# Kernel tuning notes

Measured on AMD Instinct MI355X. Metric: run time of the kernel, lower is better.

## Reference

```python
import jax, jax.numpy as jnp
import numpy as np

N_CLASSES = 10   # number of distinct private-attribute labels
DIM = 16         # PCA / GMM dimension (init arg `dim`)
SIGMA = 1.0      # init arg `sigma`, cov = sigma * I


def _pca(X, k):
    # torch PCA: center, SVD of X^T, project onto first k left singular vectors
    X = X - jnp.mean(X, axis=0)
    U, _, _ = jnp.linalg.svd(X.T, full_matrices=False)  # U: [D, min(D,B)]
    return X @ U[:, :k]                                  # [B, k]


def _gmm_loss(x, labels):
    # x: [B, k] PCA-projected features, labels: [B] int class ids in [0, C)
    B = x.shape[0]
    dtype = x.dtype
    ones = jnp.ones((B,), dtype)
    counts = jax.ops.segment_sum(ones, labels, num_segments=N_CLASSES)          # [C]
    sums = jax.ops.segment_sum(x, labels, num_segments=N_CLASSES)               # [C, k]
    safe = jnp.maximum(counts, 1.0)
    means = sums / safe[:, None]                                                # [C, k]

    diff = x - means[labels]                                                    # [B, k]
    outers = diff[:, :, None] * diff[:, None, :]                                # [B, k, k]
    Ssum = jax.ops.segment_sum(outers, labels, num_segments=N_CLASSES)          # [C, k, k]
    Sigma = SIGMA * jnp.eye(DIM, dtype=dtype) + Ssum / safe[:, None, None]      # [C, k, k]

    inv = jnp.linalg.inv(Sigma)                                                 # [C, k, k]
    _, logdet = jnp.linalg.slogdet(Sigma)                                       # [C]

    # KL(N_i || N_j) = 0.5*(tr(S_j^-1 S_i) + (u_j-u_i)^T S_j^-1 (u_j-u_i) - k + logdet_j - logdet_i)
    tr = jnp.einsum('jab,iba->ij', inv, Sigma)                                  # [C, C]
    d = means[None, :, :] - means[:, None, :]                                   # d[i,j] = u_j - u_i
    maha = jnp.einsum('ija,jab,ijb->ij', d, inv, d)                             # [C, C]
    kl = 0.5 * (tr + maha - DIM + logdet[None, :] - logdet[:, None])            # [C, C]

    present = counts > 0
    W = counts[:, None] * counts[None, :]
    mask = present[:, None] & present[None, :] & ~jnp.eye(N_CLASSES, dtype=bool)
    result = jnp.sum(jnp.where(mask, kl * W, jnp.zeros_like(kl)))
    return result / (jnp.asarray(B, dtype) ** 3)


def setup_inputs() -> dict:
    key = jax.random.key(0)
    k1, k2 = jax.random.split(key)
    mu = jax.random.normal(k1, (16384, 1024), dtype=jnp.float32)
    private_attribute = jax.random.randint(k2, (16384,), 0, N_CLASSES, dtype=jnp.int32)
    return {"mu": mu, "private_attribute": private_attribute}


def reference(mu, private_attribute):
    B = mu.shape[0]
    x = mu.reshape(B, -1)          # flatten(start_dim=1)
    x = _pca(x, DIM)               # [B, DIM]
    labels = private_attribute.astype(jnp.int32)
    return _gmm_loss(x, labels)
```

## Files before the change

kernel.cpp:

```cpp
#include <hip/hip_runtime.h>
#include <math.h>

#define BN 16384
#define DN 1024
#define CHEB_D 8

static constexpr size_t OFF_C    = 0x000000;
static constexpr size_t OFF_P    = 0x400000;
static constexpr size_t OFF_Y0   = 0x800000;
static constexpr size_t OFF_Y1   = 0x840000;
static constexpr size_t OFF_Y2   = 0x880000;
static constexpr size_t OFF_Y3   = 0x8C0000;
static constexpr size_t OFF_CQ   = 0x900000;
static constexpr size_t OFF_S64  = 0x940000;
static constexpr size_t OFF_LF   = 0x948000;
static constexpr size_t OFF_T64  = 0x950000;
static constexpr size_t OFF_V16  = 0x958000;
static constexpr size_t OFF_UT   = 0x960000;
static constexpr size_t OFF_UTT  = 0x970000;
static constexpr size_t OFF_S16  = 0x980000;
static constexpr size_t OFF_CS   = 0x980100;
static constexpr size_t OFF_TR   = 0x981100;
static constexpr size_t OFF_SCAL = 0x981200;
static constexpr size_t OFF_STAT = 0x981300;
static constexpr size_t OFF_F    = 0x990000;
static constexpr size_t OFF_M    = 0xA90000;

typedef float f32x4 __attribute__((ext_vector_type(4)));
typedef short bf16x4 __attribute__((ext_vector_type(4)));
typedef unsigned int u32x4v __attribute__((ext_vector_type(4)));


__global__ __launch_bounds__(256) void colsum_k(const float* __restrict__ X, float* __restrict__ cs){
  int b = blockIdx.x, t = threadIdx.x;
  float a0=0.f,a1=0.f,a2=0.f,a3=0.f;
  for (int r=0; r<256; ++r){
    const float4 v = *(const float4*)(X + (size_t)(b*256 + r)*1024 + t*4);
    a0 += v.x; a1 += v.y; a2 += v.z; a3 += v.w;
  }
  atomicAdd(&cs[t*4+0], a0); atomicAdd(&cs[t*4+1], a1);
  atomicAdd(&cs[t*4+2], a2); atomicAdd(&cs[t*4+3], a3);
}

#define SYRK_SLICES 27
#define SYRK_KCHUNK 608

__device__ __forceinline__ f32x4 mfma_bf16(bf16x4 a, bf16x4 b, f32x4 c){
  return __builtin_amdgcn_mfma_f32_16x16x16bf16_1k(a, b, c, 0, 0, 0);
}

__global__ __launch_bounds__(256, 2) void syrk_mfma_k(const float* __restrict__ X, float* __restrict__ G){
  int bx = blockIdx.x;
  int tp = bx % 36, ks = bx / 36;
  int ti = 0, rem = tp;
  while (rem >= 8 - ti){ rem -= 8 - ti; ++ti; }
  int tj = ti + rem;
  int k0 = ks * SYRK_KCHUNK;
  int kend = k0 + SYRK_KCHUNK; if (kend > 16384) kend = 16384;

  __shared__ __attribute__((aligned(16))) unsigned int LdsT[2][3][128][20];

  int t = threadIdx.x;
  int wid = t >> 6, lane = t & 63;
  int wr = wid >> 1, wc = wid & 1;
  int lm = lane & 15;
  int lk = lane >> 4;

  f32x4 acc[4][4];
  #pragma unroll
  for (int i=0;i<4;++i)
    #pragma unroll
    for (int j=0;j<4;++j) acc[i][j] = (f32x4){0.f,0.f,0.f,0.f};

  for (int kc = k0; kc < kend; kc += 32){
    __syncthreads();
    #pragma unroll
    for (int w=0; w<4; ++w){
      int job = t + 256*w;
      int c   = job & 127;
      int pk  = job >> 7;
      int p   = pk >> 2;
      int kpg = pk & 3;
      const float* src = X + (size_t)(kc + kpg*8)*1024 + (p ? tj : ti)*128 + c;
      float e[8];
      #pragma unroll
      for (int i=0;i<8;++i) e[i] = src[(size_t)i*1024];
      unsigned hh[8]; float r2f[8]; unsigned mm[8];
      #pragma unroll
      for (int i=0;i<8;++i){
        unsigned u = __float_as_uint(e[i]);
        hh[i] = u & 0xFFFF0000u;
        float r1 = e[i] - __uint_as_float(hh[i]);
        mm[i] = __float_as_uint(r1) & 0xFFFF0000u;
        r2f[i] = r1 - __uint_as_float(mm[i]);
      }
      u32x4v hp, mp, lp;
      #pragma unroll
      for (int j=0;j<4;++j){
        hp[j] = (hh[2*j] >> 16) | hh[2*j+1];
        mp[j] = (mm[2*j] >> 16) | mm[2*j+1];
        lp[j] = (__float_as_uint(r2f[2*j]) >> 16) | (__float_as_uint(r2f[2*j+1]) & 0xFFFF0000u);
      }
      *(u32x4v*)&LdsT[p][0][c][kpg*4] = hp;
      *(u32x4v*)&LdsT[p][1][c][kpg*4] = mp;
      *(u32x4v*)&LdsT[p][2][c][kpg*4] = lp;
    }
    __syncthreads();
    #pragma unroll
    for (int h=0; h<2; ++h){
      bf16x4 af[3][4], bg[3][4];
      #pragma unroll
      for (int fm=0; fm<4; ++fm){
        int ca = wr*64 + fm*16 + lm;
        int cb = wc*64 + fm*16 + lm;
        #pragma unroll
        for (int tm=0; tm<3; ++tm){
          af[tm][fm] = *(const bf16x4*)&LdsT[0][tm][ca][h*8 + lk*2];
          bg[tm][fm] = *(const bf16x4*)&LdsT[1][tm][cb][h*8 + lk*2];
        }
      }
      #pragma unroll
      for (int fm=0; fm<4; ++fm)
        #pragma unroll
        for (int fn=0; fn<4; ++fn){
          f32x4 a = acc[fm][fn];
          a = mfma_bf16(af[0][fm], bg[0][fn], a);
          a = mfma_bf16(af[0][fm], bg[1][fn], a);
          a = mfma_bf16(af[1][fm], bg[0][fn], a);
          a = mfma_bf16(af[0][fm], bg[2][fn], a);
          a = mfma_bf16(af[2][fm], bg[0][fn], a);
          a = mfma_bf16(af[1][fm], bg[1][fn], a);
          acc[fm][fn] = a;
        }
    }
  }
  #pragma unroll
  for (int fm=0; fm<4; ++fm){
    int gi = ti*128 + wr*64 + fm*16 + lk*4;
    #pragma unroll
    for (int fn=0; fn<4; ++fn){
      int gj = tj*128 + wc*64 + fn*16 + lm;
      #pragma unroll
      for (int rg=0; rg<4; ++rg)
        atomicAdd(&G[(size_t)(gi+rg)*1024 + gj], acc[fm][fn][rg]);
    }
  }
}

template<int KCHUNK>
__device__ __forceinline__ void syrk_body(const float* __restrict__ X, float* __restrict__ G, int KMAX){
  int bx = blockIdx.x;
  int tp = bx % 36, ks = bx / 36;
  int ti = 0, rem = tp;
  while (rem >= 8 - ti){ rem -= 8 - ti; ++ti; }
  int tj = ti + rem;
  int k0 = ks * KCHUNK;
  int kend = k0 + KCHUNK; if (kend > KMAX) kend = KMAX;
  __shared__ __attribute__((aligned(16))) float Xa[16][132];
  __shared__ __attribute__((aligned(16))) float Xb[16][132];
  int t = threadIdx.x;
  int tx = t & 15, ty = t >> 4;
  int kk0 = t >> 5, f4 = t & 31;
  const float* ba = X + (size_t)kk0*1024 + ti*128 + f4*4;
  const float* bb = X + (size_t)kk0*1024 + tj*128 + f4*4;
  float4 pa0, pa1, pb0, pb1;
  {
    size_t o = (size_t)k0*1024;
    pa0 = *(const float4*)(ba + o);
    pb0 = *(const float4*)(bb + o);
    pa1 = *(const float4*)(ba + o + 8*1024);
    pb1 = *(const float4*)(bb + o + 8*1024);
  }
  float acc[8][8];
  #pragma unroll
  for (int i=0;i<8;++i)
    #pragma unroll
    for (int j=0;j<8;++j) acc[i][j] = 0.f;
  for (int kc = k0; kc < kend; kc += 16){
    __syncthreads();
    *(float4*)&Xa[kk0][f4*4]   = pa0;
    *(float4*)&Xa[kk0+8][f4*4] = pa1;
    *(float4*)&Xb[kk0][f4*4]   = pb0;
    *(float4*)&Xb[kk0+8][f4*4] = pb1;
    __syncthreads();
    if (kc + 16 < kend){
      size_t o = (size_t)(kc+16)*1024;
      pa0 = *(const float4*)(ba + o);
      pb0 = *(const float4*)(bb + o);
      pa1 = *(const float4*)(ba + o + 8*1024);
      pb1 = *(const float4*)(bb + o + 8*1024);
    }
    #pragma unroll
    for (int kk=0; kk<16; ++kk){
      float a[8], b[8];
      *(float4*)&a[0] = *(const float4*)&Xa[kk][tx*4];
      *(float4*)&a[4] = *(const float4*)&Xa[kk][64 + tx*4];
      *(float4*)&b[0] = *(const float4*)&Xb[kk][ty*4];
      *(float4*)&b[4] = *(const float4*)&Xb[kk][64 + ty*4];
      #pragma unroll
      for (int i=0;i<8;++i)
        #pragma unroll
        for (int j=0;j<8;++j) acc[i][j] += a[i]*b[j];
    }
  }
  #pragma unroll
  for (int i=0;i<8;++i){
    int ri = ti*128 + ((i<4) ? (tx*4+i) : (64 + tx*4 + (i-4)));
    #pragma unroll
    for (int j=0;j<8;++j){
      int cj = tj*128 + ((j<4) ? (ty*4+j) : (64 + ty*4 + (j-4)));
      atomicAdd(&G[(size_t)ri*1024 + cj], acc[i][j]);
    }
  }
}

__global__ __launch_bounds__(256, 3) void syrkM_k(const float* __restrict__ X, float* __restrict__ G){
  syrk_body<128>(X, G, 1024);
}

__global__ __launch_bounds__(256) void formC_k(float* __restrict__ C, const float* __restrict__ cs, float* __restrict__ tr){
  int g = blockIdx.x*256 + threadIdx.x;
  int i = g >> 10, j = g & 1023;
  if (j < i) return;
  float v = C[g] - cs[i]*cs[j]*(1.0f/16384.0f);
  C[g] = v;
  C[j*1024 + i] = v;
  if (i == j) atomicAdd(tr, v);
}

__global__ void scal_k(const float* __restrict__ tr, float* __restrict__ scal){
  float trD = tr[0] * (1.0f/1024.0f);
  float c = 1.40f * trD, a = 0.25f * trD;
  scal[0] = 0.5f*(c + a);
  scal[1] = 2.0f/(c - a);
}

__global__ __launch_bounds__(256) void formChat_k(float* __restrict__ C, const float* __restrict__ scal){
  int g = blockIdx.x*256 + threadIdx.x;
  int i = g >> 10, j = g & 1023;
  float mid = scal[0], ie = scal[1];
  C[g] = ie*(C[g] - ((i==j) ? mid : 0.f));
}

__global__ __launch_bounds__(256) void formM_k(float* __restrict__ M){
  int g = blockIdx.x*256 + threadIdx.x;
  int i = g >> 10, j = g & 1023;
  if (j < i) return;
  float v = 2.f*M[g] - ((i==j) ? 1.f : 0.f);
  M[g] = v;
  M[j*1024 + i] = v;
}

__global__ void rng_k(float* __restrict__ Y){
  int idx = blockIdx.x*256 + threadIdx.x;
  unsigned h = (unsigned)idx * 2654435761u;
  h ^= h >> 16; h *= 2246822519u; h ^= h >> 13; h *= 3266489917u; h ^= h >> 16;
  Y[idx] = (float)(h & 0xFFFFFFu) * (2.0f/16777216.0f) - 1.0f;
}

__global__ __launch_bounds__(256) void mv_k(const float* __restrict__ Yt, const float* __restrict__ Cm, float* __restrict__ P){
  int bx = blockIdx.x;
  int nt = bx & 15, ks = bx >> 4;
  int n0 = nt*64, k0 = ks*64;
  __shared__ __attribute__((aligned(16))) float At[64][68];
  __shared__ __attribute__((aligned(16))) float Bt[64][68];
  int t = threadIdx.x;
  #pragma unroll
  for (int w=0; w<4; ++w){
    int job = t + 256*w;
    int m  = job >> 4, f4 = job & 15;
    float4 v = *(const float4*)(Yt + (size_t)m*1024 + k0 + f4*4);
    At[f4*4+0][m] = v.x; At[f4*4+1][m] = v.y; At[f4*4+2][m] = v.z; At[f4*4+3][m] = v.w;
    int kk = job >> 4, fn = job & 15;
    *(float4*)&Bt[kk][fn*4] = *(const float4*)(Cm + (size_t)(k0+kk)*1024 + n0 + fn*4);
  }
  __syncthreads();
  int tm = t & 15, tn = t >> 4;
  float acc[4][4];
  #pragma unroll
  for (int i=0;i<4;++i)
    #pragma unroll
    for (int j=0;j<4;++j) acc[i][j]=0.f;
  for (int kk=0; kk<64; ++kk){
    float4 a = *(const float4*)&At[kk][tm*4];
    float4 b = *(const float4*)&Bt[kk][tn*4];
    float av[4] = {a.x,a.y,a.z,a.w};
    float bv[4] = {b.x,b.y,b.z,b.w};
    #pragma unroll
    for (int i=0;i<4;++i)
      #pragma unroll
      for (int j=0;j<4;++j) acc[i][j] += av[i]*bv[j];
  }
  #pragma unroll
  for (int i=0;i<4;++i){
    float4 o; o.x=acc[i][0]; o.y=acc[i][1]; o.z=acc[i][2]; o.w=acc[i][3];
    *(float4*)(P + (size_t)(ks*64 + tm*4 + i)*1024 + n0 + tn*4) = o;
  }
}

__global__ __launch_bounds__(256) void combine_k(const float* __restrict__ P, const float* __restrict__ Tk1,
                                                 float* __restrict__ out, int mode){
  int idx = (blockIdx.x*256 + threadIdx.x)*4;
  float s0=0.f,s1=0.f,s2=0.f,s3=0.f;
  #pragma unroll
  for (int ks=0; ks<16; ++ks){
    const float4 p = *(const float4*)(P + (size_t)ks*65536 + idx);
    s0 += p.x; s1 += p.y; s2 += p.z; s3 += p.w;
  }
  float4 o;
  if (mode == 0){
    o.x=s0; o.y=s1; o.z=s2; o.w=s3;
  } else {
    const float4 t1 = *(const float4*)(Tk1 + idx);
    o.x = 2.f*s0 - t1.x; o.y = 2.f*s1 - t1.y;
    o.z = 2.f*s2 - t1.z; o.w = 2.f*s3 - t1.w;
  }
  *(float4*)(out+idx) = o;
}

__global__ __launch_bounds__(256) void gram_k(const float* __restrict__ A, const float* __restrict__ Bm, double* __restrict__ S){
  int bx = blockIdx.x;
  int i = bx >> 2, jg = bx & 3;
  __shared__ __attribute__((aligned(16))) float Ai[1024];
  __shared__ double red[16][17];
  int t = threadIdx.x;
  ((float4*)Ai)[t] = ((const float4*)(A + (size_t)i*1024))[t];
  __syncthreads();
  int jl = t >> 4, kp = t & 15;
  const float* Br = Bm + (size_t)(jg*16 + jl)*1024 + kp*64;
  const float* Ar = Ai + kp*64;
  double acc = 0.0;
  #pragma unroll 8
  for (int kk=0; kk<64; ++kk) acc += (double)Br[kk] * (double)Ar[kk];
  red[jl][kp] = acc;
  __syncthreads();
  if (t < 16){
    double s = 0.0;
    #pragma unroll
    for (int p2=0; p2<16; ++p2) s += red[t][p2];
    S[i*64 + jg*16 + t] = s;
  }
}

__global__ __launch_bounds__(64) void chol_k(const double* __restrict__ S, float* __restrict__ Lf){
  __shared__ double L[64][65];
  __shared__ double col[64];
  int t = threadIdx.x;
  for (int e=t; e<4096; e+=64) L[e>>6][e&63] = S[e];
  __syncthreads();
  for (int k=0; k<64; ++k){
    double lkk = sqrt(fmax(L[k][k], 1e-280));
    double r = 1.0/lkk;
    double ck = (t > k) ? L[t][k]*r : 0.0;
    col[t] = ck;
    if (t == k) L[k][k] = lkk;
    if (t > k)  L[t][k] = ck;
    __syncthreads();
    #pragma unroll
    for (int j=0; j<64; j+=8){
      L[t][j+0] -= ck*col[j+0];
      L[t][j+1] -= ck*col[j+1];
      L[t][j+2] -= ck*col[j+2];
      L[t][j+3] -= ck*col[j+3];
      L[t][j+4] -= ck*col[j+4];
      L[t][j+5] -= ck*col[j+5];
      L[t][j+6] -= ck*col[j+6];
      L[t][j+7] -= ck*col[j+7];
    }
    __syncthreads();
  }
  for (int e=t; e<4096; e+=64){
    int i = e >> 6, j = e & 63;
    Lf[e] = (j < i) ? (float)L[i][j] : ((j == i) ? (float)(1.0/L[i][i]) : 0.f);
  }
}

__global__ __launch_bounds__(256) void applysolve_k(const float* __restrict__ Yin, const float* __restrict__ Lf, float* __restrict__ Qout){
  int k = blockIdx.x*256 + threadIdx.x;
  float z[64];
  #pragma unroll
  for (int c=0; c<64; ++c){
    float v = Yin[(size_t)c*1024 + k];
    #pragma unroll
    for (int j=0; j<c; ++j) v -= Lf[c*64+j]*z[j];
    z[c] = v * Lf[c*64+c];
  }
  #pragma unroll
  for (int c=0; c<64; ++c) Qout[(size_t)c*1024 + k] = z[c];
}

__device__ __forceinline__ float wsumf(float v){
  #pragma unroll
  for (int off=32; off; off>>=1) v += __shfl_xor(v, off, 64);
  return v;
}
__device__ __forceinline__ float wminf(float v){
  #pragma unroll
  for (int off=32; off; off>>=1) v = fminf(v, __shfl_xor(v, off, 64));
  return v;
}
__device__ __forceinline__ float wmaxf(float v){
  #pragma unroll
  for (int off=32; off; off>>=1) v = fmaxf(v, __shfl_xor(v, off, 64));
  return v;
}
__device__ __forceinline__ float lanebc(float x, int l){
  return __int_as_float(__builtin_amdgcn_readlane(__float_as_int(x), l));
}

__global__ __launch_bounds__(256) void eig16_k(const double* __restrict__ Tin, float* __restrict__ V16){
  __shared__ float A[64][65];
  __shared__ float pp[4][64];
  __shared__ float dF[64], eF[64], e2F[64], kapS[64];
  __shared__ float lamF[16];
  __shared__ float IV[5][64][16];
  __shared__ float W[16][68];
  int t = threadIdx.x;
  int r = t & 63, p4 = t >> 6;
  int j0 = p4*16;

  for (int e=t; e<4096; e+=256){
    int i = e >> 6, j = e & 63;
    A[i][j] = (float)(0.5*(Tin[i*64+j] + Tin[(size_t)j*64+i]));
  }
  __syncthreads();

  for (int k=0; k<62; ++k){
    float ckreg = A[r][k];
    float ck = (r > k) ? ckreg : 0.f;
    float sig = wsumf(ck*ck);
    float x1 = lanebc(ckreg, k+1);
    float rr = sqrtf(sig);
    float alpha = (x1 >= 0.f) ? -rr : rr;
    float kappa = sig - alpha*x1;
    float kinv = (kappa > 1e-30f) ? 1.f/kappa : 0.f;
    float vown = ck;
    if (r == k+1) vown = x1 - alpha;
    if (kinv == 0.f) vown = 0.f;
    if (t == 0){ eF[k] = (kinv==0.f) ? 0.f : alpha; kapS[k] = (kinv==0.f) ? 0.f : kappa; }
    float vj[16];
    #pragma unroll
    for (int jj=0; jj<16; ++jj){
      int j = j0 + jj;
      float cj = lanebc(ckreg, j);
      float vv = (j > k) ? cj : 0.f;
      if (j == k+1) vv = x1 - alpha;
      if (kinv == 0.f) vv = 0.f;
      vj[jj] = vv;
    }
    float prt = 0.f;
    #pragma unroll
    for (int jj=0; jj<16; ++jj) prt += A[r][j0+jj]*vj[jj];
    pp[p4][r] = prt;
    __syncthreads();
    float pfull = pp[0][r] + pp[1][r] + pp[2][r] + pp[3][r];
    float pi = (r > k) ? pfull*kinv : 0.f;
    float vp = wsumf(vown*pi);
    float Kc = vp*0.5f*kinv;
    float qown = (r > k) ? (pi - Kc*vown) : 0.f;
    #pragma unroll
    for (int jj=0; jj<16; ++jj){
      int j = j0 + jj;
      float qj = lanebc(qown, j);
      float aold = A[r][j];
      float anew = aold - (vown*qj + qown*vj[jj]);
      if (j == k) anew = (r > k) ? vown : aold;
      A[r][j] = anew;
    }
    __syncthreads();
  }

  if (t < 64) dF[t] = A[t][t];
  if (t == 0){ eF[62] = A[63][62]; eF[63] = 0.f; kapS[62] = 0.f; kapS[63] = 0.f; }
  __syncthreads();
  if (t < 64) e2F[t] = eF[t]*eF[t];
  __syncthreads();

  float em1 = (r > 0) ? fabsf(eF[r-1]) : 0.f;
  float ep  = fabsf(eF[r]);
  float glo = wminf(dF[r] - em1 - ep);
  float ghi = wmaxf(dF[r] + em1 + ep);
  float span = ghi - glo + 1.f;
  float lo = glo - 0.001f*span, hi = ghi + 0.001f*span;

  int eidx = t >> 4, g = t & 15;
  int m = 48 + eidx;
  for (int it=0; it<7; ++it){
    float x = lo + (hi - lo)*((float)(g+1)*(1.0f/17.0f));
    float qq = dF[0] - x;
    int c = (qq < 0.f) ? 1 : 0;
    #pragma unroll
    for (int j=1; j<64; ++j){
      float aq = fabsf(qq);
      float qs = (aq < 1e-10f) ? ((qq < 0.f) ? -1e-10f : 1e-10f) : qq;
      qq = dF[j] - x - e2F[j-1]*__builtin_amdgcn_rcpf(qs);
      c += (qq < 0.f) ? 1 : 0;
    }
    float cl = (c <= m) ? x : -3.4e38f;
    float ch = (c >  m) ? x :  3.4e38f;
    #pragma unroll
    for (int off=1; off<16; off<<=1){
      cl = fmaxf(cl, __shfl_xor(cl, off, 64));
      ch = fminf(ch, __shfl_xor(ch, off, 64));
    }
    lo = fmaxf(lo, cl);
    hi = fminf(hi, ch);
  }
  if (g == 0) lamF[eidx] = 0.5f*(lo + hi);
  __syncthreads();

  if (t < 16){
    float lam = lamF[t];
    const float PIVF = 1e-6f;
    #pragma unroll 4
    for (int i=0; i<64; ++i){
      unsigned hsh = (unsigned)(i*131 + t*1009 + 7);
      hsh ^= hsh >> 13; hsh *= 2654435761u; hsh ^= hsh >> 16;
      IV[4][i][t] = (float)(hsh & 0xFFFF) * (1.5f/65536.0f) + 0.25f;
    }
    unsigned long long piv = 0ull;
    float dcur = dF[0] - lam;
    float ducur = eF[0];
    for (int i=0; i<63; ++i){
      float dli = eF[i];
      float dnext = dF[i+1] - lam;
      float eip1 = (i < 62) ? eF[i+1] : 0.f;
      bool sw = fabsf(dcur) < fabsf(dli);
      float dd = dcur;
      if (fabsf(dd) < PIVF) dd = (dd < 0.f) ? -PIVF : PIVF;
      float f = sw ? (dcur*__builtin_amdgcn_rcpf(dli)) : (dli*__builtin_amdgcn_rcpf(dd));
      float ddst = sw ? dli : dd;
      float dust = sw ? dnext : ducur;
      float du2  = sw ? eip1 : 0.f;
      float dnew = sw ? (ducur - f*dnext) : (dnext - f*ducur);
      float dunew= sw ? (-f*eip1) : eip1;
      if (sw) piv |= (1ull << i);
      IV[0][i][t] = f;
      float dc = ddst; if (fabsf(dc) < PIVF) dc = (dc < 0.f) ? -PIVF : PIVF;
      IV[1][i][t] = __builtin_amdgcn_rcpf(dc);
      IV[2][i][t] = dust;
      IV[3][i][t] = du2;
      dcur = dnew; ducur = dunew;
    }
    { float dc = dcur; if (fabsf(dc) < PIVF) dc = (dc < 0.f) ? -PIVF : PIVF; IV[1][63][t] = __builtin_amdgcn_rcpf(dc); }
    float ss = 0.f;
    #pragma unroll 1
    for (int iter=0; iter<2; ++iter){
      float scale = (iter == 0) ? 1.f : rsqrtf(fmaxf(ss, 1e-30f));
      float b = IV[4][0][t]*scale;
      #pragma unroll 7
      for (int i=0; i<63; ++i){
        float bn = IV[4][i+1][t]*scale;
        float f = IV[0][i][t];
        bool sw = (piv >> i) & 1ull;
        float keep = sw ? bn : b;
        float bnew = (sw ? b : bn) - f*keep;
        IV[4][i][t] = keep;
        b = bnew;
      }
      ss = 0.f;
      float x1v = b * IV[1][63][t];
      IV[4][63][t] = x1v; ss += x1v*x1v;
      float x0v = (IV[4][62][t] - IV[2][62][t]*x1v) * IV[1][62][t];
      IV[4][62][t] = x0v; ss += x0v*x0v;
      float xp1 = x0v, xp2 = x1v;
      #pragma unroll 7
      for (int i=61; i>=0; --i){
        float xi = (IV[4][i][t] - IV[2][i][t]*xp1 - IV[3][i][t]*xp2) * IV[1][i][t];
        IV[4][i][t] = xi; ss += xi*xi;
        xp2 = xp1; xp1 = xi;
      }
    }
    #pragma unroll 4
    for (int i=0; i<64; ++i) W[t][i] = IV[4][i][t];
  }
  __syncthreads();

  for (int c=0; c<16; ++c){
    float wi = (t < 64) ? W[c][t] : 0.f;
    float s2 = wsumf(wi*wi);
    float rn = rsqrtf(fmaxf(s2, 1e-30f));
    wi *= rn;
    if (t < 64) W[c][t] = wi;
    __syncthreads();
    for (int c2=c+1; c2<16; ++c2){
      float w2 = (t < 64) ? W[c2][t] : 0.f;
      float d2 = wsumf(wi*w2);
      if (t < 64) W[c2][t] -= d2*wi;
    }
    __syncthreads();
  }

  int cL = (p4 << 2) + (r >> 4);
  int part = r & 15;
  for (int k=61; k>=0; --k){
    float kpd = kapS[k];
    if (kpd == 0.f) continue;
    float invk = 1.f/kpd;
    float vv[4];
    float ps = 0.f;
    #pragma unroll
    for (int mm=0; mm<4; ++mm){
      int i = part*4 + mm;
      vv[mm] = (i > k) ? A[i][k] : 0.f;
      ps += vv[mm]*W[cL][i];
    }
    ps += __shfl_xor(ps, 1, 64);
    ps += __shfl_xor(ps, 2, 64);
    ps += __shfl_xor(ps, 4, 64);
    ps += __shfl_xor(ps, 8, 64);
    float sc = ps * invk;
    #pragma unroll
    for (int mm=0; mm<4; ++mm){
      int i = part*4 + mm;
      W[cL][i] -= vv[mm]*sc;
    }
  }
  __syncthreads();

  for (int e=t; e<1024; e+=256){
    int j = e >> 4, c = e & 15;
    V16[e] = W[c][j];
  }
}

__global__ __launch_bounds__(256) void buildUt_k(const float* __restrict__ V16,
                                                 const float* __restrict__ Qt, float* __restrict__ Ut, float* __restrict__ UtT){
  int bx = blockIdx.x;
  int c = bx & 15, kc = bx >> 4;
  int k = kc*256 + threadIdx.x;
  float acc = 0.f;
  #pragma unroll
  for (int j=0; j<64; ++j) acc += V16[j*16 + c] * Qt[(size_t)j*1024 + k];
  Ut[(size_t)c*1024 + k] = acc;
  UtT[(size_t)k*16 + c] = acc;
}

__global__ void s16_k(const float* __restrict__ cs, const float* __restrict__ Ut, float* __restrict__ s16){
  __shared__ float red[16][17];
  int t = threadIdx.x;
  int c = t & 15, part = t >> 4;
  float acc = 0.f;
  for (int d=0; d<64; ++d) acc += cs[part*64 + d] * Ut[(size_t)c*1024 + part*64 + d];
  red[c][part] = acc;
  __syncthreads();
  if (t < 16){
    float s = 0.f;
    #pragma unroll
    for (int p2=0; p2<16; ++p2) s += red[t][p2];
    s16[t] = s * (1.0f/16384.0f);
  }
}

__global__ __launch_bounds__(256) void proj_k(const float* __restrict__ X, const float* __restrict__ UtT,
                                              const float* __restrict__ s16, float* __restrict__ F){
  int r0 = blockIdx.x * 64;
  int t = threadIdx.x;
  __shared__ __attribute__((aligned(16))) float uts[16384];
  #pragma unroll
  for (int w=0; w<16; ++w)
    ((float4*)uts)[t + 256*w] = ((const float4*)UtT)[t + 256*w];
  __syncthreads();
  int row = t & 63, kp = t >> 6;
  const float* xr = X + (size_t)(r0 + row)*1024 + kp*256;
  const float* ut = uts + kp*256*16;
  float acc[16];
  #pragma unroll
  for (int c=0;c<16;++c) acc[c] = 0.f;
  for (int dd=0; dd<256; dd+=4){
    float4 xv4 = *(const float4*)(xr + dd);
    float xv[4] = {xv4.x, xv4.y, xv4.z, xv4.w};
    #pragma unroll
    for (int u=0; u<4; ++u)
      #pragma unroll
      for (int c=0;c<16;++c) acc[c] += xv[u] * ut[(dd+u)*16 + c];
  }
  __shared__ float part[4][64][16];
  #pragma unroll
  for (int c=0;c<16;++c) part[kp][row][c] = acc[c];
  __syncthreads();
  int cq = t >> 6;
  #pragma unroll
  for (int ccx=0; ccx<4; ++ccx){
    int c = cq*4 + ccx;
    float v = part[0][row][c] + part[1][row][c] + part[2][row][c] + part[3][row][c] - s16[c];
    F[(size_t)(r0 + row)*16 + c] = v;
  }
}

__global__ __launch_bounds__(256) void stats_k(const float* __restrict__ F, const int* __restrict__ lbl, float* __restrict__ SG){
  __shared__ float st[10][154];
  int t = threadIdx.x;
  for (int e=t; e<1540; e+=256) st[e/154][e%154] = 0.f;
  __syncthreads();
  int r = blockIdx.x*256 + t;
  float f[16];
  #pragma unroll
  for (int w=0; w<4; ++w){
    float4 v = *(const float4*)(F + (size_t)r*16 + w*4);
    f[w*4+0]=v.x; f[w*4+1]=v.y; f[w*4+2]=v.z; f[w*4+3]=v.w;
  }
  int c = lbl[r];
  if ((unsigned)c < 10u){
    float* bs = &st[c][0];
    atomicAdd(&bs[0], 1.f);
    #pragma unroll
    for (int a=0;a<16;++a) atomicAdd(&bs[1+a], f[a]);
    int sidx = 17;
    #pragma unroll
    for (int a=0;a<16;++a)
      #pragma unroll
      for (int b2=a;b2<16;++b2) atomicAdd(&bs[sidx++], f[a]*f[b2]);
  }
  __syncthreads();
  for (int e=t; e<1530; e+=256) atomicAdd(&SG[e], st[e/153][e%153]);
}

__global__ __launch_bounds__(256) void final_k(const float* __restrict__ SG, float* __restrict__ out){
  __shared__ double cnt[10], safe[10], ldet[10];
  __shared__ double mean[10][16];
  __shared__ double Sig[10][16][16];
  __shared__ double Inv[10][16][16];
  __shared__ double red[128];
  int t = threadIdx.x;
  if (t < 10){
    double c0 = (double)SG[t*153];
    cnt[t] = c0; safe[t] = (c0 > 0.0) ? c0 : 1.0;
  }
  __syncthreads();
  for (int e=t; e<160; e+=256){
    int c = e >> 4, a = e & 15;
    mean[c][a] = (double)SG[c*153 + 1 + a] / safe[c];
  }
  __syncthreads();
  for (int e=t; e<2560; e+=256){
    int c = e >> 8, ab = e & 255, a = ab >> 4, b2 = ab & 15;
    int lo = a < b2 ? a : b2, hi = a < b2 ? b2 : a;
    int ti = lo*(33 - lo)/2 + (hi - lo);
    Sig[c][a][b2] = (double)SG[c*153 + 17 + ti]/safe[c] - mean[c][a]*mean[c][b2] + ((a==b2)?1.0:0.0);
  }
  __syncthreads();
  if (t < 10){
    for (int a=0;a<16;++a)
      for (int b2=0;b2<16;++b2) Inv[t][a][b2] = Sig[t][a][b2];
    double ld2 = 0.0;
    for (int k=0;k<16;++k){
      double v = Inv[t][k][k];
      for (int j=0;j<k;++j) v -= Inv[t][k][j]*Inv[t][k][j];
      v = fmax(v, 1e-280);
      double lkk = sqrt(v);
      Inv[t][k][k] = lkk; ld2 += log(lkk);
      for (int i=k+1;i<16;++i){
        double w = Inv[t][i][k];
        for (int j=0;j<k;++j) w -= Inv[t][i][j]*Inv[t][k][j];
        Inv[t][i][k] = w / lkk;
      }
    }
    ldet[t] = 2.0*ld2;
    for (int j=0;j<16;++j){
      double dj = 1.0 / Inv[t][j][j];
      Inv[t][j][j] = dj;
      for (int i=j+1;i<16;++i){
        double ssum = Inv[t][i][j]*dj;
        for (int k=j+1;k<i;++k) ssum += Inv[t][i][k]*Inv[t][k][j];
        Inv[t][i][j] = -ssum / Inv[t][i][i];
      }
    }
    double dg[16];
    #pragma unroll
    for (int a=0;a<16;++a){
      double s2 = 0.0;
      for (int k=a;k<16;++k){ double x = Inv[t][k][a]; s2 += x*x; }
      dg[a] = s2;
    }
    for (int a=0;a<16;++a)
      for (int b2=a+1;b2<16;++b2){
        double s2 = 0.0;
        for (int k=b2;k<16;++k) s2 += Inv[t][k][a]*Inv[t][k][b2];
        Inv[t][a][b2] = s2;
      }
    for (int a=0;a<16;++a) Inv[t][a][a] = dg[a];
    for (int a=0;a<16;++a)
      for (int b2=a+1;b2<16;++b2) Inv[t][b2][a] = Inv[t][a][b2];
  }
  __syncthreads();
  double contrib = 0.0;
  if (t < 100){
    int i = t/10, j = t%10;
    if (i != j && cnt[i] > 0.0 && cnt[j] > 0.0){
      double tr = 0.0;
      for (int a=0;a<16;++a)
        for (int b2=0;b2<16;++b2) tr += Inv[j][a][b2]*Sig[i][b2][a];
      double dm[16];
      #pragma unroll
      for (int a=0;a<16;++a) dm[a] = mean[j][a] - mean[i][a];
      double mah = 0.0;
      for (int a=0;a<16;++a){
        double rs = 0.0;
        for (int b2=0;b2<16;++b2) rs += Inv[j][a][b2]*dm[b2];
        mah += dm[a]*rs;
      }
      double kl = 0.5*(tr + mah - 16.0 + ldet[j] - ldet[i]);
      contrib = kl * cnt[i]*cnt[j];
    }
  }
  if (t < 128) red[t] = contrib;
  __syncthreads();
  for (int off=64; off>0; off >>= 1){
    if (t < off) red[t] += red[t+off];
    __syncthreads();
  }
  if (t == 0) out[0] = (float)(red[0] / (16384.0*16384.0*16384.0));
}

extern "C" void kernel_launch(void* const* d_in, const int* in_sizes, int n_in,
                              void* d_out, int out_size, void* d_ws, size_t ws_size,
                              hipStream_t stream){
  (void)in_sizes; (void)n_in; (void)out_size; (void)ws_size;
  const float* X  = (const float*)d_in[0];
  const int* lbl  = (const int*)d_in[1];
  char* ws = (char*)d_ws;
  float*  C    = (float*)(ws + OFF_C);
  float*  Mm   = (float*)(ws + OFF_M);
  float*  P    = (float*)(ws + OFF_P);
  float*  Y0   = (float*)(ws + OFF_Y0);
  float*  Y1   = (float*)(ws + OFF_Y1);
  float*  Y2   = (float*)(ws + OFF_Y2);
  float*  Y3   = (float*)(ws + OFF_Y3);
  float*  CQ   = (float*)(ws + OFF_CQ);
  double* S64  = (double*)(ws + OFF_S64);
  float*  LF   = (float*)(ws + OFF_LF);
  double* T64  = (double*)(ws + OFF_T64);
  float*  V16  = (float*)(ws + OFF_V16);
  float*  UT   = (float*)(ws + OFF_UT);
  float*  UTT  = (float*)(ws + OFF_UTT);
  float*  S16  = (float*)(ws + OFF_S16);
  float*  CS   = (float*)(ws + OFF_CS);
  float*  TRC  = (float*)(ws + OFF_TR);
  float*  SCAL = (float*)(ws + OFF_SCAL);
  float*  STAT = (float*)(ws + OFF_STAT);
  float*  F    = (float*)(ws + OFF_F);
  float*  OUT  = (float*)d_out;

  hipMemsetAsync(C, 0, 4*1024*1024, stream);
  hipMemsetAsync(Mm, 0, 4*1024*1024, stream);
  hipMemsetAsync(ws + OFF_CS, 0, 12800, stream);

  colsum_k<<<64, 256, 0, stream>>>(X, CS);
  syrk_mfma_k<<<36*SYRK_SLICES, 256, 0, stream>>>(X, C);
  formC_k<<<4096, 256, 0, stream>>>(C, CS, TRC);
  scal_k<<<1, 1, 0, stream>>>(TRC, SCAL);
  formChat_k<<<4096, 256, 0, stream>>>(C, SCAL);
  syrkM_k<<<36*8, 256, 0, stream>>>(C, Mm);
  formM_k<<<4096, 256, 0, stream>>>(Mm);
  rng_k<<<256, 256, 0, stream>>>(Y0);

  auto cheb = [&](float* in, float* z0, float* z1, float* z2) -> float* {
    float* bufs[3] = {z0, z1, z2};
    float* prev = in;
    float* cur = in;
    for (int s=0; s<CHEB_D; ++s){
      float* dst = bufs[s % 3];
      mv_k<<<256, 256, 0, stream>>>(cur, Mm, P);
      combine_k<<<64, 256, 0, stream>>>(P, prev, dst, (s == 0) ? 0 : 1);
      prev = cur; cur = dst;
    }
    return cur;
  };
  auto cholqr = [&](float* Yin, float* Qout){
    gram_k<<<256, 256, 0, stream>>>(Yin, Yin, S64);
    chol_k<<<1, 64, 0, stream>>>(S64, LF);
    applysolve_k<<<4, 256, 0, stream>>>(Yin, LF, Qout);
  };

  float* f1 = cheb(Y0, Y1, Y2, Y3);
  cholqr(f1, Y0);
  float* f2 = cheb(Y0, Y1, Y2, Y3);
  cholqr(f2, Y1);
  cholqr(Y1, Y3);

  mv_k<<<256, 256, 0, stream>>>(Y3, Mm, P);
  combine_k<<<64, 256, 0, stream>>>(P, Y3, CQ, 0);
  gram_k<<<256, 256, 0, stream>>>(Y3, CQ, T64);
  eig16_k<<<1, 256, 0, stream>>>(T64, V16);
  buildUt_k<<<64, 256, 0, stream>>>(V16, Y3, UT, UTT);

  s16_k<<<1, 256, 0, stream>>>(CS, UT, S16);
  proj_k<<<256, 256, 0, stream>>>(X, UTT, S16, F);
  stats_k<<<64, 256, 0, stream>>>(F, lbl, STAT);
  final_k<<<1, 256, 0, stream>>>(STAT, OUT);
}
```

Baseline: 1.348 ms.

## Use 16x16x32 bf16 MFMA, MFMA-based second SYRK, fuse centering and shift

Switches the split-bf16 SYRK to the wider 16x16x32 bf16 MFMA, which consumes a full 32-wide k chunk per instruction instead of two halves. The second SYRK (C·C for M) moves from a scalar FP32 FMA kernel to the same 3-term bf16-split MFMA body with its own k slicing. The trace is computed directly from the diagonal in a small reduction kernel, which lets centering and Chebyshev shift/scale fuse into one elementwise pass and drops one full 4 MB pass plus the atomic trace. The bf16x3 split on the second product can lose accuracy relative to plain FP32.

```diff
diff --git a/kernel.cpp b/kernel.cpp
--- a/kernel.cpp
+++ b/kernel.cpp
@@ -27,8 +27,27 @@
 static constexpr size_t OFF_M    = 0xA90000;
 
 typedef float f32x4 __attribute__((ext_vector_type(4)));
-typedef short bf16x4 __attribute__((ext_vector_type(4)));
+typedef short bf16x8 __attribute__((ext_vector_type(8)));
 typedef unsigned int u32x4v __attribute__((ext_vector_type(4)));
+
+__device__ __forceinline__ float wsumf(float v){
+  #pragma unroll
+  for (int off=32; off; off>>=1) v += __shfl_xor(v, off, 64);
+  return v;
+}
+__device__ __forceinline__ float wminf(float v){
+  #pragma unroll
+  for (int off=32; off; off>>=1) v = fminf(v, __shfl_xor(v, off, 64));
+  return v;
+}
+__device__ __forceinline__ float wmaxf(float v){
+  #pragma unroll
+  for (int off=32; off; off>>=1) v = fmaxf(v, __shfl_xor(v, off, 64));
+  return v;
+}
+__device__ __forceinline__ float lanebc(float x, int l){
+  return __int_as_float(__builtin_amdgcn_readlane(__float_as_int(x), l));
+}
 
 
 __global__ __launch_bounds__(256) void colsum_k(const float* __restrict__ X, float* __restrict__ cs){
@@ -44,19 +63,22 @@
 
 #define SYRK_SLICES 27
 #define SYRK_KCHUNK 608
-
-__device__ __forceinline__ f32x4 mfma_bf16(bf16x4 a, bf16x4 b, f32x4 c){
-  return __builtin_amdgcn_mfma_f32_16x16x16bf16_1k(a, b, c, 0, 0, 0);
-}
-
-__global__ __launch_bounds__(256, 2) void syrk_mfma_k(const float* __restrict__ X, float* __restrict__ G){
+#define SYRKM_SLICES 4
+#define SYRKM_KCHUNK 256
+
+__device__ __forceinline__ f32x4 mfma32(bf16x8 a, bf16x8 b, f32x4 c){
+  return __builtin_amdgcn_mfma_f32_16x16x32_bf16(a, b, c, 0, 0, 0);
+}
+
+template<int KCHUNK>
+__device__ __forceinline__ void syrk_mfma_body(const float* __restrict__ X, float* __restrict__ G, int KMAX){
   int bx = blockIdx.x;
   int tp = bx % 36, ks = bx / 36;
   int ti = 0, rem = tp;
   while (rem >= 8 - ti){ rem -= 8 - ti; ++ti; }
   int tj = ti + rem;
-  int k0 = ks * SYRK_KCHUNK;
-  int kend = k0 + SYRK_KCHUNK; if (kend > 16384) kend = 16384;
+  int k0 = ks * KCHUNK;
+  int kend = k0 + KCHUNK; if (kend > KMAX) kend = KMAX;
 
   __shared__ __attribute__((aligned(16))) unsigned int LdsT[2][3][128][20];
 
@@ -106,33 +128,30 @@
       *(u32x4v*)&LdsT[p][2][c][kpg*4] = lp;
     }
     __syncthreads();
-    #pragma unroll
-    for (int h=0; h<2; ++h){
-      bf16x4 af[3][4], bg[3][4];
-      #pragma unroll
-      for (int fm=0; fm<4; ++fm){
-        int ca = wr*64 + fm*16 + lm;
-        int cb = wc*64 + fm*16 + lm;
-        #pragma unroll
-        for (int tm=0; tm<3; ++tm){
-          af[tm][fm] = *(const bf16x4*)&LdsT[0][tm][ca][h*8 + lk*2];
-          bg[tm][fm] = *(const bf16x4*)&LdsT[1][tm][cb][h*8 + lk*2];
-        }
-      }
-      #pragma unroll
-      for (int fm=0; fm<4; ++fm)
-        #pragma unroll
-        for (int fn=0; fn<4; ++fn){
-          f32x4 a = acc[fm][fn];
-          a = mfma_bf16(af[0][fm], bg[0][fn], a);
-          a = mfma_bf16(af[0][fm], bg[1][fn], a);
-          a = mfma_bf16(af[1][fm], bg[0][fn], a);
-          a = mfma_bf16(af[0][fm], bg[2][fn], a);
-          a = mfma_bf16(af[2][fm], bg[0][fn], a);
-          a = mfma_bf16(af[1][fm], bg[1][fn], a);
-          acc[fm][fn] = a;
-        }
-    }
+    bf16x8 af[3][4], bg[3][4];
+    #pragma unroll
+    for (int fm=0; fm<4; ++fm){
+      int ca = wr*64 + fm*16 + lm;
+      int cb = wc*64 + fm*16 + lm;
+      #pragma unroll
+      for (int tm=0; tm<3; ++tm){
+        af[tm][fm] = *(const bf16x8*)&LdsT[0][tm][ca][lk*4];
+        bg[tm][fm] = *(const bf16x8*)&LdsT[1][tm][cb][lk*4];
+      }
+    }
+    #pragma unroll
+    for (int fm=0; fm<4; ++fm)
+      #pragma unroll
+      for (int fn=0; fn<4; ++fn){
+        f32x4 a = acc[fm][fn];
+        a = mfma32(af[0][fm], bg[0][fn], a);
+        a = mfma32(af[0][fm], bg[1][fn], a);
+        a = mfma32(af[1][fm], bg[0][fn], a);
+        a = mfma32(af[0][fm], bg[2][fn], a);
+        a = mfma32(af[2][fm], bg[0][fn], a);
+        a = mfma32(af[1][fm], bg[1][fn], a);
+        acc[fm][fn] = a;
+      }
   }
   #pragma unroll
   for (int fm=0; fm<4; ++fm){
@@ -147,99 +166,45 @@
   }
 }
 
-template<int KCHUNK>
-__device__ __forceinline__ void syrk_body(const float* __restrict__ X, float* __restrict__ G, int KMAX){
-  int bx = blockIdx.x;
-  int tp = bx % 36, ks = bx / 36;
-  int ti = 0, rem = tp;
-  while (rem >= 8 - ti){ rem -= 8 - ti; ++ti; }
-  int tj = ti + rem;
-  int k0 = ks * KCHUNK;
-  int kend = k0 + KCHUNK; if (kend > KMAX) kend = KMAX;
-  __shared__ __attribute__((aligned(16))) float Xa[16][132];
-  __shared__ __attribute__((aligned(16))) float Xb[16][132];
-  int t = threadIdx.x;
-  int tx = t & 15, ty = t >> 4;
-  int kk0 = t >> 5, f4 = t & 31;
-  const float* ba = X + (size_t)kk0*1024 + ti*128 + f4*4;
-  const float* bb = X + (size_t)kk0*1024 + tj*128 + f4*4;
-  float4 pa0, pa1, pb0, pb1;
-  {
-    size_t o = (size_t)k0*1024;
-    pa0 = *(const float4*)(ba + o);
-    pb0 = *(const float4*)(bb + o);
-    pa1 = *(const float4*)(ba + o + 8*1024);
-    pb1 = *(const float4*)(bb + o + 8*1024);
-  }
-  float acc[8][8];
-  #pragma unroll
-  for (int i=0;i<8;++i)
-    #pragma unroll
-    for (int j=0;j<8;++j) acc[i][j] = 0.f;
-  for (int kc = k0; kc < kend; kc += 16){
-    __syncthreads();
-    *(float4*)&Xa[kk0][f4*4]   = pa0;
-    *(float4*)&Xa[kk0+8][f4*4] = pa1;
-    *(float4*)&Xb[kk0][f4*4]   = pb0;
-    *(float4*)&Xb[kk0+8][f4*4] = pb1;
-    __syncthreads();
-    if (kc + 16 < kend){
-      size_t o = (size_t)(kc+16)*1024;
-      pa0 = *(const float4*)(ba + o);
-      pb0 = *(const float4*)(bb + o);
-      pa1 = *(const float4*)(ba + o + 8*1024);
-      pb1 = *(const float4*)(bb + o + 8*1024);
-    }
-    #pragma unroll
-    for (int kk=0; kk<16; ++kk){
-      float a[8], b[8];
-      *(float4*)&a[0] = *(const float4*)&Xa[kk][tx*4];
-      *(float4*)&a[4] = *(const float4*)&Xa[kk][64 + tx*4];
-      *(float4*)&b[0] = *(const float4*)&Xb[kk][ty*4];
-      *(float4*)&b[4] = *(const float4*)&Xb[kk][64 + ty*4];
-      #pragma unroll
-      for (int i=0;i<8;++i)
-        #pragma unroll
-        for (int j=0;j<8;++j) acc[i][j] += a[i]*b[j];
-    }
-  }
-  #pragma unroll
-  for (int i=0;i<8;++i){
-    int ri = ti*128 + ((i<4) ? (tx*4+i) : (64 + tx*4 + (i-4)));
-    #pragma unroll
-    for (int j=0;j<8;++j){
-      int cj = tj*128 + ((j<4) ? (ty*4+j) : (64 + ty*4 + (j-4)));
-      atomicAdd(&G[(size_t)ri*1024 + cj], acc[i][j]);
-    }
-  }
-}
-
-__global__ __launch_bounds__(256, 3) void syrkM_k(const float* __restrict__ X, float* __restrict__ G){
-  syrk_body<128>(X, G, 1024);
-}
-
-__global__ __launch_bounds__(256) void formC_k(float* __restrict__ C, const float* __restrict__ cs, float* __restrict__ tr){
+__global__ __launch_bounds__(256, 2) void syrk_mfma_k(const float* __restrict__ X, float* __restrict__ G){
+  syrk_mfma_body<SYRK_KCHUNK>(X, G, 16384);
+}
+__global__ __launch_bounds__(256, 2) void syrkM_mfma_k(const float* __restrict__ X, float* __restrict__ G){
+  syrk_mfma_body<SYRKM_KCHUNK>(X, G, 1024);
+}
+
+__global__ __launch_bounds__(256) void trace_k(const float* __restrict__ G, const float* __restrict__ cs,
+                                               float* __restrict__ scal){
+  __shared__ float red[4];
+  int t = threadIdx.x;
+  float s = 0.f;
+  #pragma unroll
+  for (int w=0; w<4; ++w){
+    int i = t + 256*w;
+    float d = cs[i];
+    s += G[(size_t)i*1025] - d*d*(1.0f/16384.0f);
+  }
+  s = wsumf(s);
+  if ((t & 63) == 0) red[t >> 6] = s;
+  __syncthreads();
+  if (t == 0){
+    float trD = (red[0]+red[1]+red[2]+red[3]) * (1.0f/1024.0f);
+    float c = 1.40f * trD, a = 0.25f * trD;
+    scal[0] = 0.5f*(c + a);
+    scal[1] = 2.0f/(c - a);
+  }
+}
+
+__global__ __launch_bounds__(256) void formCChat_k(float* __restrict__ C, const float* __restrict__ cs,
+                                                   const float* __restrict__ scal){
   int g = blockIdx.x*256 + threadIdx.x;
   int i = g >> 10, j = g & 1023;
   if (j < i) return;
+  float mid = scal[0], ie = scal[1];
   float v = C[g] - cs[i]*cs[j]*(1.0f/16384.0f);
-  C[g] = v;
-  C[j*1024 + i] = v;
-  if (i == j) atomicAdd(tr, v);
-}
-
-__global__ void scal_k(const float* __restrict__ tr, float* __restrict__ scal){
-  float trD = tr[0] * (1.0f/1024.0f);
-  float c = 1.40f * trD, a = 0.25f * trD;
-  scal[0] = 0.5f*(c + a);
-  scal[1] = 2.0f/(c - a);
-}
-
-__global__ __launch_bounds__(256) void formChat_k(float* __restrict__ C, const float* __restrict__ scal){
-  int g = blockIdx.x*256 + threadIdx.x;
-  int i = g >> 10, j = g & 1023;
-  float mid = scal[0], ie = scal[1];
-  C[g] = ie*(C[g] - ((i==j) ? mid : 0.f));
+  float h = ie*(v - ((i==j) ? mid : 0.f));
+  C[g] = h;
+  C[j*1024 + i] = h;
 }
 
 __global__ __launch_bounds__(256) void formM_k(float* __restrict__ M){
@@ -387,25 +352,6 @@
   }
   #pragma unroll
   for (int c=0; c<64; ++c) Qout[(size_t)c*1024 + k] = z[c];
-}
-
-__device__ __forceinline__ float wsumf(float v){
-  #pragma unroll
-  for (int off=32; off; off>>=1) v += __shfl_xor(v, off, 64);
-  return v;
-}
-__device__ __forceinline__ float wminf(float v){
-  #pragma unroll
-  for (int off=32; off; off>>=1) v = fminf(v, __shfl_xor(v, off, 64));
-  return v;
-}
-__device__ __forceinline__ float wmaxf(float v){
-  #pragma unroll
-  for (int off=32; off; off>>=1) v = fmaxf(v, __shfl_xor(v, off, 64));
-  return v;
-}
-__device__ __forceinline__ float lanebc(float x, int l){
-  return __int_as_float(__builtin_amdgcn_readlane(__float_as_int(x), l));
 }
 
 __global__ __launch_bounds__(256) void eig16_k(const double* __restrict__ Tin, float* __restrict__ V16){
@@ -836,7 +782,6 @@
   float*  UTT  = (float*)(ws + OFF_UTT);
   float*  S16  = (float*)(ws + OFF_S16);
   float*  CS   = (float*)(ws + OFF_CS);
-  float*  TRC  = (float*)(ws + OFF_TR);
   float*  SCAL = (float*)(ws + OFF_SCAL);
   float*  STAT = (float*)(ws + OFF_STAT);
   float*  F    = (float*)(ws + OFF_F);
@@ -848,10 +793,9 @@
 
   colsum_k<<<64, 256, 0, stream>>>(X, CS);
   syrk_mfma_k<<<36*SYRK_SLICES, 256, 0, stream>>>(X, C);
-  formC_k<<<4096, 256, 0, stream>>>(C, CS, TRC);
-  scal_k<<<1, 1, 0, stream>>>(TRC, SCAL);
-  formChat_k<<<4096, 256, 0, stream>>>(C, SCAL);
-  syrkM_k<<<36*8, 256, 0, stream>>>(C, Mm);
+  trace_k<<<1, 256, 0, stream>>>(C, CS, SCAL);
+  formCChat_k<<<4096, 256, 0, stream>>>(C, CS, SCAL);
+  syrkM_mfma_k<<<36*SYRKM_SLICES, 256, 0, stream>>>(C, Mm);
   formM_k<<<4096, 256, 0, stream>>>(Mm);
   rng_k<<<256, 256, 0, stream>>>(Y0);
 
```

New measurement: 1.265 ms. -6.2%, faster.
